# Performance work log

Measured on AMD Instinct MI355X. Metric: run time of the kernel, lower is better.

The kernel has to match this reference:

```python
import jax, jax.numpy as jnp
from jax import lax
import numpy as np

NPOINT = 2048
NSAMPLE = 16
LEAKY = 0.1


def _leaky(x):
    return jnp.where(x >= 0, x, LEAKY * x)


def _fps(pts, npoint):
    # pts: [B, N, 3] -> idx [B, npoint] (furthest point sampling, start at index 0)
    B, N, _ = pts.shape

    def step(carry, _):
        dist, far = carry  # dist [B,N], far [B]
        c = jnp.take_along_axis(pts, far[:, None, None], axis=1)  # [B,1,3]
        d = jnp.sum((pts - c) ** 2, -1)  # [B,N]
        dist = jnp.minimum(dist, d)
        nxt = jnp.argmax(dist, -1).astype(jnp.int32)
        return (dist, nxt), far

    init = (jnp.full((B, N), 1e10, pts.dtype), jnp.zeros((B,), jnp.int32))
    _, idx = lax.scan(step, init, None, length=npoint)
    return jnp.transpose(idx)  # [B, npoint]


def setup_inputs() -> dict:
    key = jax.random.key(0)
    ks = jax.random.split(key, 6)
    B, N, D, O = 8, 8192, 64, 128
    xyz = jax.random.normal(ks[0], (B, 3, N), jnp.float32)
    points = jax.random.normal(ks[1], (B, D, N), jnp.float32)
    W_kernel = jax.random.normal(ks[2], (O, D + 3), jnp.float32) * 0.05
    W_linear = jax.random.normal(ks[3], (O + NSAMPLE, O + NSAMPLE), jnp.float32) * 0.05
    W_point = jax.random.normal(ks[4], (NSAMPLE, NSAMPLE), jnp.float32) * 0.05
    W_channel = jax.random.normal(ks[5], (O, O), jnp.float32) * 0.05
    return {"xyz": xyz, "points": points, "W_kernel": W_kernel,
            "W_linear": W_linear, "W_point": W_point, "W_channel": W_channel}


def reference(xyz, points, W_kernel, W_linear, W_point, W_channel):
    K, S = NSAMPLE, NPOINT
    xyz_t = jnp.transpose(xyz, (0, 2, 1))      # [B,N,3]
    pts_t = jnp.transpose(points, (0, 2, 1))   # [B,N,D]

    fps_idx = _fps(xyz_t, S)                   # [B,S]
    new_xyz = jax.vmap(lambda p, i: p[i])(xyz_t, fps_idx)  # [B,S,3]

    # KNN: squared distances new_xyz -> xyz
    d = (jnp.sum(new_xyz ** 2, -1)[:, :, None]
         + jnp.sum(xyz_t ** 2, -1)[:, None, :]
         - 2.0 * jnp.einsum('bsc,bnc->bsn', new_xyz, xyz_t))  # [B,S,N]
    _, knn = lax.top_k(-d, K)                  # [B,S,K]

    gxyz = jax.vmap(lambda p, i: p[i])(xyz_t, knn)          # [B,S,K,3]
    gxyz_n = gxyz - new_xyz[:, :, None, :]
    gpts = jax.vmap(lambda p, i: p[i])(pts_t, knn)          # [B,S,K,D]
    new_points = jnp.concatenate([gxyz_n, gpts], -1)        # [B,S,K,3+D]

    # 1x1 conv2d kernel + LeakyReLU
    feat = _leaky(jnp.einsum('oc,bskc->bosk', W_kernel, new_points))  # [B,O,S,K]

    ch_avg = jnp.mean(feat, -1)                # [B,O,S]
    pt_avg = jnp.mean(feat, 1)                 # [B,S,K]
    agg = jnp.concatenate([ch_avg, jnp.transpose(pt_avg, (0, 2, 1))], 1)  # [B,O+K,S]
    agg = _leaky(jnp.einsum('oc,bcs->bos', W_linear, agg))

    wp = jax.nn.sigmoid(jnp.einsum('oc,bcs->bos', W_point, agg[:, -K:]))   # [B,K,S]
    wc = jax.nn.sigmoid(jnp.einsum('oc,bcs->bos', W_channel, agg[:, :-K]))  # [B,O,S]

    gated = feat * wc[:, :, :, None] * jnp.transpose(wp, (0, 2, 1))[:, None, :, :]
    out = jnp.mean(gated, -1)                  # [B,O,S]
    return jnp.transpose(new_xyz, (0, 2, 1)), out, fps_idx
```

## Files before the change

kernel.cpp:

```cpp
#include <hip/hip_runtime.h>
#include <stdint.h>

#define NB 8
#define NPT 8192
#define ND 64
#define NO 128
#define NS 2048
#define NK 16
#define NCONS 248
#define NITER 67

typedef float f32x2 __attribute__((ext_vector_type(2)));

constexpr int WS_PTS_T  = 0;
constexpr int WS_XYZW   = WS_PTS_T + NB*NPT*ND;
constexpr int WS_GFAR   = WS_XYZW + NB*NPT*4;
constexpr int WS_SYNC   = WS_GFAR + NB*NS;

constexpr int OUT_NEWXYZ = 0;
constexpr int OUT_FEAT   = NB*3*NS;
constexpr int OUT_FPS    = OUT_FEAT + NB*NO*NS;

__device__ __forceinline__ float sq3(float x, float y, float z) {
#pragma clang fp contract(off)
  return (x*x + y*y) + z*z;
}

__device__ __forceinline__ f32x2 fps_d2(f32x2 px, f32x2 py, f32x2 pz, f32x2 cx, f32x2 cy, f32x2 cz) {
#pragma clang fp contract(off)
  f32x2 dx = px - cx, dy = py - cy, dz = pz - cz;
  return (dx*dx + dy*dy) + dz*dz;
}

__device__ __forceinline__ float knn_d(float qn, float pn,
                                       float qx,float qy,float qz,
                                       float px,float py,float pz) {
#pragma clang fp contract(off)
  float dot = (qx*px + qy*py) + qz*pz;
  return (qn + pn) - 2.0f*dot;
}

#define DPP_STEP_F(x, ctrl, rm, bm, op) { \
  int _v = __builtin_amdgcn_update_dpp(__float_as_int(x), __float_as_int(x), ctrl, rm, bm, false); \
  x = op(x, __int_as_float(_v)); }

__device__ __forceinline__ float wave_max_dpp(float x) {
  DPP_STEP_F(x, 0x111, 0xF, 0xF, fmaxf)
  DPP_STEP_F(x, 0x112, 0xF, 0xF, fmaxf)
  DPP_STEP_F(x, 0x114, 0xF, 0xF, fmaxf)
  DPP_STEP_F(x, 0x118, 0xF, 0xF, fmaxf)
  DPP_STEP_F(x, 0x142, 0xA, 0xF, fmaxf)
  DPP_STEP_F(x, 0x143, 0xC, 0xF, fmaxf)
  return x;
}
__device__ __forceinline__ float dpp8_max(float x) {
  DPP_STEP_F(x, 0x111, 0xF, 0xF, fmaxf)
  DPP_STEP_F(x, 0x112, 0xF, 0xF, fmaxf)
  DPP_STEP_F(x, 0x114, 0xF, 0xF, fmaxf)
  return x;
}

__global__ void k_init(float* __restrict__ ws) {
  int idx = blockIdx.x*512 + threadIdx.x;
  if (idx < NB*NS) ((int*)(ws + WS_GFAR))[idx] = -1;
  if (idx < 32)    ((int*)(ws + WS_SYNC))[idx] = 0;
}

struct MegaShared {
  union {
    struct {
      float lxyz[NPT][4];
      unsigned long long wred[2][8];
      int tag[2][8];
    } f;
    struct { float tile[64][65]; } tr;
    struct {
      float W[128*69];
      union {
        float dist[NPT];
        struct { float np[16*69]; float ft[16*132]; float chred[256]; float ptred[16*17]; } p2;
      } u;
      unsigned long long kred[8];
      int selIdx[16];
      float agg[144];
      float a2[144];
      float gates[144];
      int farSlot;
    } c;
  } u;
};

__global__ __launch_bounds__(512) void k_mega(const float* __restrict__ xyz,
                                              const float* __restrict__ points,
                                              const float* __restrict__ Wkern,
                                              const float* __restrict__ Wlin,
                                              const float* __restrict__ Wpt,
                                              const float* __restrict__ Wch,
                                              float* __restrict__ ws,
                                              float* __restrict__ dout) {
  __shared__ MegaShared sh;
  const int bid = blockIdx.x, t = threadIdx.x;
  int* syncp = (int*)(ws + WS_SYNC);
  int* gfar  = (int*)(ws + WS_GFAR);

  if (bid < NB) {
    const float* xb = xyz + (size_t)bid*3*NPT;
    f32x2 px2[8], py2[8], pz2[8], dist2[8];
    const int base = t << 4;
    const int w = t >> 6;
#pragma unroll
    for (int jj = 0; jj < 4; jj++) {
      float4 vx = *reinterpret_cast<const float4*>(xb + base + jj*4);
      float4 vy = *reinterpret_cast<const float4*>(xb + NPT + base + jj*4);
      float4 vz = *reinterpret_cast<const float4*>(xb + 2*NPT + base + jj*4);
      px2[jj*2+0] = f32x2{vx.x, vx.y}; px2[jj*2+1] = f32x2{vx.z, vx.w};
      py2[jj*2+0] = f32x2{vy.x, vy.y}; py2[jj*2+1] = f32x2{vy.z, vy.w};
      pz2[jj*2+0] = f32x2{vz.x, vz.y}; pz2[jj*2+1] = f32x2{vz.z, vz.w};
      dist2[jj*2+0] = f32x2{1e10f, 1e10f}; dist2[jj*2+1] = f32x2{1e10f, 1e10f};
      float xs[4] = {vx.x, vx.y, vx.z, vx.w};
      float ys[4] = {vy.x, vy.y, vy.z, vy.w};
      float zs[4] = {vz.x, vz.y, vz.z, vz.w};
#pragma unroll
      for (int i = 0; i < 4; i++) {
        float4 rec; rec.x = xs[i]; rec.y = ys[i]; rec.z = zs[i]; rec.w = 0.f;
        *reinterpret_cast<float4*>(&sh.u.f.lxyz[base + jj*4 + i][0]) = rec;
      }
    }
    if (t < 16) sh.u.f.tag[t >> 3][t & 7] = 0;
    __syncthreads();

    int far = 0;
    int* gfb = gfar + (size_t)bid*NS;

    for (int s = 0; s < NS; s++) {
      if (t == 0)
        __hip_atomic_store(&gfb[s], far, __ATOMIC_RELAXED, __HIP_MEMORY_SCOPE_AGENT);

      const float4 c4 = *reinterpret_cast<const float4*>(&sh.u.f.lxyz[far][0]);
      const f32x2 c2x = {c4.x, c4.x}, c2y = {c4.y, c4.y}, c2z = {c4.z, c4.z};

      f32x2 vmax2 = {-1.0f, -1.0f};
#pragma unroll
      for (int j = 0; j < 8; j++) {
        f32x2 dd = fps_d2(px2[j], py2[j], pz2[j], c2x, c2y, c2z);
        f32x2 nd;
        nd.x = fminf(dist2[j].x, dd.x);
        nd.y = fminf(dist2[j].y, dd.y);
        dist2[j] = nd;
        vmax2.x = fmaxf(vmax2.x, nd.x);
        vmax2.y = fmaxf(vmax2.y, nd.y);
      }
      float bv = fmaxf(vmax2.x, vmax2.y);
      int bi = base;
#pragma unroll
      for (int j = 7; j >= 0; --j) {
        if (dist2[j].y == bv) bi = base + 2*j + 1;
        if (dist2[j].x == bv) bi = base + 2*j;
      }
      float wm = wave_max_dpp(bv);
      float wmax = __int_as_float(__builtin_amdgcn_readlane(__float_as_int(wm), 63));
      unsigned long long eq = __ballot(bv == wmax);
      int winner = __ffsll((unsigned long long)eq) - 1;
      int wbi = __builtin_amdgcn_readlane(bi, winner);

      const int par = s & 1;
      const int mytag = (s >> 1) + 1;
      if ((t & 63) == 0) {
        sh.u.f.wred[par][w] = ((unsigned long long)__float_as_uint(wmax) << 32) | (unsigned)wbi;
        __hip_atomic_store(&sh.u.f.tag[par][w], mytag, __ATOMIC_RELEASE, __HIP_MEMORY_SCOPE_WORKGROUP);
      }
      {
        int* tp = &sh.u.f.tag[par][t & 7];
        while (__hip_atomic_load(tp, __ATOMIC_ACQUIRE, __HIP_MEMORY_SCOPE_WORKGROUP) != mytag) {}
      }
      {
        unsigned long long kk = sh.u.f.wred[par][t & 7];
        float sv = __int_as_float((int)(unsigned)(kk >> 32));
        float sm = dpp8_max(sv);
        float M = __int_as_float(__builtin_amdgcn_readlane(__float_as_int(sm), 7));
        unsigned long long eqm = __ballot(sv == M) & 0xFFull;
        int wwin = __ffsll(eqm) - 1;
        far = __builtin_amdgcn_readlane((int)(kk & 0xFFFFFFFFull), wwin);
      }
    }
    return;
  }

  const int cbid = bid - NB;

  for (int tile = cbid; tile < 1024; tile += NCONS) {
    const int b  = tile >> 7;
    const int n0 = (tile & 127) << 6;
    const float* pb = points + (size_t)b*ND*NPT;
    {
      int dR = t >> 3, cg = t & 7;
      const float* src = pb + (size_t)dR*NPT + n0 + cg*8;
      float4 v0 = *reinterpret_cast<const float4*>(src);
      float4 v1 = *reinterpret_cast<const float4*>(src + 4);
      sh.u.tr.tile[dR][cg*8+0]=v0.x; sh.u.tr.tile[dR][cg*8+1]=v0.y;
      sh.u.tr.tile[dR][cg*8+2]=v0.z; sh.u.tr.tile[dR][cg*8+3]=v0.w;
      sh.u.tr.tile[dR][cg*8+4]=v1.x; sh.u.tr.tile[dR][cg*8+5]=v1.y;
      sh.u.tr.tile[dR][cg*8+6]=v1.z; sh.u.tr.tile[dR][cg*8+7]=v1.w;
    }
    __syncthreads();
    {
      int nl = t >> 3, dg = t & 7;
      float4 w0, w1;
      w0.x = sh.u.tr.tile[dg*8+0][nl]; w0.y = sh.u.tr.tile[dg*8+1][nl];
      w0.z = sh.u.tr.tile[dg*8+2][nl]; w0.w = sh.u.tr.tile[dg*8+3][nl];
      w1.x = sh.u.tr.tile[dg*8+4][nl]; w1.y = sh.u.tr.tile[dg*8+5][nl];
      w1.z = sh.u.tr.tile[dg*8+6][nl]; w1.w = sh.u.tr.tile[dg*8+7][nl];
      float* dst = ws + WS_PTS_T + ((size_t)b*NPT + n0 + nl)*ND + dg*8;
      *reinterpret_cast<float4*>(dst)     = w0;
      *reinterpret_cast<float4*>(dst + 4) = w1;
    }
    __syncthreads();
  }
  for (int chunk = cbid; chunk < 128; chunk += NCONS) {
    int g = chunk*512 + t;
    int b = g >> 13, n = g & 8191;
    const float* xb = xyz + (size_t)b*3*NPT;
    float x = xb[n], y = xb[NPT+n], z = xb[2*NPT+n];
    float4 v; v.x=x; v.y=y; v.z=z; v.w=sq3(x,y,z);
    *reinterpret_cast<float4*>(ws + WS_XYZW + (size_t)g*4) = v;
  }
  __syncthreads();
  if (t == 0) {
    __hip_atomic_fetch_add(&syncp[0], 1, __ATOMIC_ACQ_REL, __HIP_MEMORY_SCOPE_AGENT);
    while (__hip_atomic_load(&syncp[0], __ATOMIC_RELAXED, __HIP_MEMORY_SCOPE_AGENT) < NCONS)
      __builtin_amdgcn_s_sleep(8);
    (void)__hip_atomic_load(&syncp[0], __ATOMIC_ACQUIRE, __HIP_MEMORY_SCOPE_AGENT);
  }
  __syncthreads();

  for (int g = t; g < 128*67; g += 512) {
    int o = g / 67, c = g - o*67;
    sh.u.c.W[o*69+c] = Wkern[g];
  }
  __syncthreads();

  for (int j = 0; j < NITER; j++) {
    const int i = cbid + j*NCONS;
    const bool active = (i < NB*NS);
    const int ii = active ? i : (NB*NS - 1);
    const int b = ii & 7, s = ii >> 3;

    if (t == 0) {
      int f;
      while ((f = __hip_atomic_load(&gfar[(size_t)b*NS + s], __ATOMIC_RELAXED, __HIP_MEMORY_SCOPE_AGENT)) == -1)
        __builtin_amdgcn_s_sleep(8);
      sh.u.c.farSlot = f;
    }
    __syncthreads();
    const int far = sh.u.c.farSlot;

    const float* xyzw = ws + WS_XYZW + (size_t)b*NPT*4;
    const float4 q = *reinterpret_cast<const float4*>(xyzw + (size_t)far*4);

    if (active) {
      if (t == 3) dout[OUT_FPS + (size_t)b*NS + s] = (float)far;
      else if (t < 3) dout[OUT_NEWXYZ + (size_t)b*3*NS + (size_t)t*NS + s] = (t==0) ? q.x : (t==1) ? q.y : q.z;
    }

#pragma unroll
    for (int i2 = 0; i2 < 16; i2++) {
      int n = t + (i2 << 9);
      float4 p = *reinterpret_cast<const float4*>(xyzw + (size_t)n*4);
      sh.u.c.u.dist[n] = knn_d(q.w, p.w, q.x, q.y, q.z, p.x, p.y, p.z);
    }
    __syncthreads();

    for (int r = 0; r < NK; r++) {
      float bv = __int_as_float(0x7F800000); int bi = NPT;
#pragma unroll
      for (int i2 = 0; i2 < 16; i2++) {
        int n = t + (i2 << 9);
        float v = sh.u.c.u.dist[n];
        if (v < bv) { bv = v; bi = n; }
      }
      unsigned uu = __float_as_uint(bv);
      uu ^= ((unsigned)((int)uu >> 31)) | 0x80000000u;
      unsigned long long key = ((unsigned long long)uu << 32) | (unsigned)bi;
#pragma unroll
      for (int m = 1; m < 64; m <<= 1) {
        unsigned long long o = __shfl_xor(key, m, 64);
        key = (o < key) ? o : key;
      }
      if ((t & 63) == 0) sh.u.c.kred[t >> 6] = key;
      __syncthreads();
      if (t == 0) {
        unsigned long long kmin = sh.u.c.kred[0];
#pragma unroll
        for (int w2 = 1; w2 < 8; w2++) { unsigned long long o = sh.u.c.kred[w2]; if (o < kmin) kmin = o; }
        int win = (int)(kmin & 0xFFFFFFFFull);
        sh.u.c.selIdx[r] = win;
        sh.u.c.u.dist[win] = __int_as_float(0x7F800000);
      }
      __syncthreads();
    }

    if (t < 256) {
      int k = t >> 4, cg = t & 15;
      int idx = sh.u.c.selIdx[k];
      float4 f = *reinterpret_cast<const float4*>(ws + WS_PTS_T + ((size_t)b*NPT + idx)*ND + cg*4);
      float* nprow = sh.u.c.u.p2.np + k*69;
      nprow[3+cg*4+0]=f.x; nprow[3+cg*4+1]=f.y; nprow[3+cg*4+2]=f.z; nprow[3+cg*4+3]=f.w;
      if (cg == 0) {
        float4 g4 = *reinterpret_cast<const float4*>(xyzw + (size_t)idx*4);
        nprow[0]=g4.x-q.x; nprow[1]=g4.y-q.y; nprow[2]=g4.z-q.z;
      }
    }
    __syncthreads();

    if (t < 256) {
      const int o = t & 127, khalf = t >> 7, k0 = khalf*8;
      float acc[8] = {0,0,0,0,0,0,0,0};
      const float* Wrow = sh.u.c.W + o*69;
      for (int c = 0; c < 67; c++) {
        float wv = Wrow[c];
#pragma unroll
        for (int kk = 0; kk < 8; kk++)
          acc[kk] = fmaf(wv, sh.u.c.u.p2.np[(k0+kk)*69 + c], acc[kk]);
      }
      float chp = 0.f;
#pragma unroll
      for (int kk = 0; kk < 8; kk++) {
        float a = acc[kk]; a = (a >= 0.f) ? a : 0.1f*a;
        sh.u.c.u.p2.ft[(k0+kk)*132 + o] = a; chp += a;
      }
      sh.u.c.u.p2.chred[khalf*128 + o] = chp;
    }
    __syncthreads();

    if (t < 128) sh.u.c.agg[t] = (sh.u.c.u.p2.chred[t] + sh.u.c.u.p2.chred[128+t]) * 0.0625f;
    if (t < 256) {
      int k = t & 15, og = t >> 4;
      float pp = 0.f;
#pragma unroll
      for (int jj = 0; jj < 8; jj++) pp += sh.u.c.u.p2.ft[k*132 + og*8 + jj];
      sh.u.c.u.p2.ptred[k*17 + og] = pp;
    }
    __syncthreads();
    if (t < 16) {
      float pv = 0.f;
#pragma unroll
      for (int og = 0; og < 16; og++) pv += sh.u.c.u.p2.ptred[t*17 + og];
      sh.u.c.agg[128 + t] = pv * 0.0078125f;
    }
    __syncthreads();

    if (t < 144) {
      float a = 0.f;
      const float* wr = Wlin + t*144;
      for (int c = 0; c < 144; c++) a = fmaf(wr[c], sh.u.c.agg[c], a);
      sh.u.c.a2[t] = (a >= 0.f) ? a : 0.1f*a;
    }
    __syncthreads();

    if (t < 128) {
      float a = 0.f;
      const float* wr = Wch + t*128;
      for (int c = 0; c < 128; c++) a = fmaf(wr[c], sh.u.c.a2[c], a);
      sh.u.c.gates[t] = 1.f / (1.f + expf(-a));
    } else if (t < 144) {
      int o = t - 128;
      float a = 0.f;
      const float* wr = Wpt + o*16;
      for (int c = 0; c < 16; c++) a = fmaf(wr[c], sh.u.c.a2[128+c], a);
      sh.u.c.gates[t] = 1.f / (1.f + expf(-a));
    }
    __syncthreads();

    if (t < 128 && active) {
      float sum = 0.f;
#pragma unroll
      for (int k = 0; k < 16; k++)
        sum = fmaf(sh.u.c.u.p2.ft[k*132 + t], sh.u.c.gates[128 + k], sum);
      dout[OUT_FEAT + ((size_t)b*NO + t)*NS + s] = sum * sh.u.c.gates[t] * 0.0625f;
    }
    __syncthreads();
  }
}

extern "C" void kernel_launch(void* const* d_in, const int* in_sizes, int n_in,
                              void* d_out, int out_size, void* d_ws, size_t ws_size,
                              hipStream_t stream) {
  (void)in_sizes; (void)n_in; (void)out_size; (void)ws_size;
  const float* xyz    = (const float*)d_in[0];
  const float* points = (const float*)d_in[1];
  const float* Wk     = (const float*)d_in[2];
  const float* Wl     = (const float*)d_in[3];
  const float* Wp     = (const float*)d_in[4];
  const float* Wc     = (const float*)d_in[5];
  float* ws  = (float*)d_ws;
  float* out = (float*)d_out;

  hipLaunchKernelGGL(k_init, dim3(32), dim3(512), 0, stream, ws);

  void* args[] = { (void*)&xyz, (void*)&points, (void*)&Wk, (void*)&Wl,
                   (void*)&Wp, (void*)&Wc, (void*)&ws, (void*)&out };
  hipLaunchCooperativeKernel(reinterpret_cast<void*>(k_mega),
                             dim3(NB + NCONS), dim3(512), args, 0, stream);
}
```

Measured before the change: 1.992 ms.

## Streamline KNN top-k reduction and replace FPS tag spin with barrier

```diff
diff --git a/kernel.cpp b/kernel.cpp
--- a/kernel.cpp
+++ b/kernel.cpp
@@ -43,6 +43,9 @@
 #define DPP_STEP_F(x, ctrl, rm, bm, op) { \
   int _v = __builtin_amdgcn_update_dpp(__float_as_int(x), __float_as_int(x), ctrl, rm, bm, false); \
   x = op(x, __int_as_float(_v)); }
+#define DPP_STEP_U(x, ctrl, rm, cmp) { \
+  unsigned _v = (unsigned)__builtin_amdgcn_update_dpp((int)x, (int)x, ctrl, rm, 0xF, false); \
+  x = (_v cmp x) ? _v : x; }
 
 __device__ __forceinline__ float wave_max_dpp(float x) {
   DPP_STEP_F(x, 0x111, 0xF, 0xF, fmaxf)
@@ -53,6 +56,20 @@
   DPP_STEP_F(x, 0x143, 0xC, 0xF, fmaxf)
   return x;
 }
+__device__ __forceinline__ float wave_min_dpp(float x) {
+  DPP_STEP_F(x, 0x111, 0xF, 0xF, fminf)
+  DPP_STEP_F(x, 0x112, 0xF, 0xF, fminf)
+  DPP_STEP_F(x, 0x114, 0xF, 0xF, fminf)
+  DPP_STEP_F(x, 0x118, 0xF, 0xF, fminf)
+  DPP_STEP_F(x, 0x142, 0xA, 0xF, fminf)
+  DPP_STEP_F(x, 0x143, 0xC, 0xF, fminf)
+  return x;
+}
+__device__ __forceinline__ unsigned wave_umin_dpp(unsigned x) {
+  DPP_STEP_U(x, 0x111, 0xF, <) DPP_STEP_U(x, 0x112, 0xF, <) DPP_STEP_U(x, 0x114, 0xF, <)
+  DPP_STEP_U(x, 0x118, 0xF, <) DPP_STEP_U(x, 0x142, 0xA, <) DPP_STEP_U(x, 0x143, 0xC, <)
+  return x;
+}
 __device__ __forceinline__ float dpp8_max(float x) {
   DPP_STEP_F(x, 0x111, 0xF, 0xF, fmaxf)
   DPP_STEP_F(x, 0x112, 0xF, 0xF, fmaxf)
@@ -71,7 +88,6 @@
     struct {
       float lxyz[NPT][4];
       unsigned long long wred[2][8];
-      int tag[2][8];
     } f;
     struct { float tile[64][65]; } tr;
     struct {
@@ -80,8 +96,7 @@
         float dist[NPT];
         struct { float np[16*69]; float ft[16*132]; float chred[256]; float ptred[16*17]; } p2;
       } u;
-      unsigned long long kred[8];
-      int selIdx[16];
+      unsigned long long kred[2][8];
       float agg[144];
       float a2[144];
       float gates[144];
@@ -107,7 +122,6 @@
     const float* xb = xyz + (size_t)bid*3*NPT;
     f32x2 px2[8], py2[8], pz2[8], dist2[8];
     const int base = t << 4;
-    const int w = t >> 6;
 #pragma unroll
     for (int jj = 0; jj < 4; jj++) {
       float4 vx = *reinterpret_cast<const float4*>(xb + base + jj*4);
@@ -126,7 +140,6 @@
         *reinterpret_cast<float4*>(&sh.u.f.lxyz[base + jj*4 + i][0]) = rec;
       }
     }
-    if (t < 16) sh.u.f.tag[t >> 3][t & 7] = 0;
     __syncthreads();
 
     int far = 0;
@@ -162,17 +175,10 @@
       unsigned long long eq = __ballot(bv == wmax);
       int winner = __ffsll((unsigned long long)eq) - 1;
       int wbi = __builtin_amdgcn_readlane(bi, winner);
-
       const int par = s & 1;
-      const int mytag = (s >> 1) + 1;
-      if ((t & 63) == 0) {
-        sh.u.f.wred[par][w] = ((unsigned long long)__float_as_uint(wmax) << 32) | (unsigned)wbi;
-        __hip_atomic_store(&sh.u.f.tag[par][w], mytag, __ATOMIC_RELEASE, __HIP_MEMORY_SCOPE_WORKGROUP);
-      }
-      {
-        int* tp = &sh.u.f.tag[par][t & 7];
-        while (__hip_atomic_load(tp, __ATOMIC_ACQUIRE, __HIP_MEMORY_SCOPE_WORKGROUP) != mytag) {}
-      }
+      if ((t & 63) == 0)
+        sh.u.f.wred[par][t >> 6] = ((unsigned long long)__float_as_uint(wmax) << 32) | (unsigned)wbi;
+      __syncthreads();
       {
         unsigned long long kk = sh.u.f.wred[par][t & 7];
         float sv = __int_as_float((int)(unsigned)(kk >> 32));
@@ -239,6 +245,8 @@
   }
   __syncthreads();
 
+  const int myK = t >> 4;
+
   for (int j = 0; j < NITER; j++) {
     const int i = cbid + j*NCONS;
     const bool active = (i < NB*NS);
@@ -270,38 +278,43 @@
     }
     __syncthreads();
 
+    int exclWin = NPT;
+    int myIdx = 0;
     for (int r = 0; r < NK; r++) {
       float bv = __int_as_float(0x7F800000); int bi = NPT;
 #pragma unroll
       for (int i2 = 0; i2 < 16; i2++) {
         int n = t + (i2 << 9);
         float v = sh.u.c.u.dist[n];
-        if (v < bv) { bv = v; bi = n; }
-      }
-      unsigned uu = __float_as_uint(bv);
-      uu ^= ((unsigned)((int)uu >> 31)) | 0x80000000u;
-      unsigned long long key = ((unsigned long long)uu << 32) | (unsigned)bi;
-#pragma unroll
-      for (int m = 1; m < 64; m <<= 1) {
-        unsigned long long o = __shfl_xor(key, m, 64);
-        key = (o < key) ? o : key;
-      }
-      if ((t & 63) == 0) sh.u.c.kred[t >> 6] = key;
+        if (n != exclWin && v < bv) { bv = v; bi = n; }
+      }
+      float wmv = wave_min_dpp(bv);
+      float M = __int_as_float(__builtin_amdgcn_readlane(__float_as_int(wmv), 63));
+      unsigned cand = (bv == M) ? (unsigned)bi : 0xFFFFFFFFu;
+      unsigned wcv = wave_umin_dpp(cand);
+      unsigned widx = (unsigned)__builtin_amdgcn_readlane((int)wcv, 63);
+      if ((t & 63) == 0)
+        sh.u.c.kred[r & 1][t >> 6] = ((unsigned long long)__float_as_uint(M) << 32) | widx;
       __syncthreads();
-      if (t == 0) {
-        unsigned long long kmin = sh.u.c.kred[0];
-#pragma unroll
-        for (int w2 = 1; w2 < 8; w2++) { unsigned long long o = sh.u.c.kred[w2]; if (o < kmin) kmin = o; }
-        int win = (int)(kmin & 0xFFFFFFFFull);
-        sh.u.c.selIdx[r] = win;
-        sh.u.c.u.dist[win] = __int_as_float(0x7F800000);
-      }
-      __syncthreads();
+      unsigned long long k0 = sh.u.c.kred[r & 1][0];
+      float best = __int_as_float((int)(unsigned)(k0 >> 32));
+      unsigned bidx = (unsigned)(k0 & 0xFFFFFFFFull);
+#pragma unroll
+      for (int w2 = 1; w2 < 8; w2++) {
+        unsigned long long kk = sh.u.c.kred[r & 1][w2];
+        float v2 = __int_as_float((int)(unsigned)(kk >> 32));
+        unsigned ix = (unsigned)(kk & 0xFFFFFFFFull);
+        if (v2 < best || (v2 == best && ix < bidx)) { best = v2; bidx = ix; }
+      }
+      const int win = (int)bidx;
+      if (r == myK) myIdx = win;
+      if (r < NK-1 && (win & 511) == t) sh.u.c.u.dist[win] = __int_as_float(0x7F800000);
+      exclWin = win;
     }
 
     if (t < 256) {
-      int k = t >> 4, cg = t & 15;
-      int idx = sh.u.c.selIdx[k];
+      int k = myK, cg = t & 15;
+      int idx = myIdx;
       float4 f = *reinterpret_cast<const float4*>(ws + WS_PTS_T + ((size_t)b*NPT + idx)*ND + cg*4);
       float* nprow = sh.u.c.u.p2.np + k*69;
       nprow[3+cg*4+0]=f.x; nprow[3+cg*4+1]=f.y; nprow[3+cg*4+2]=f.z; nprow[3+cg*4+3]=f.w;
@@ -313,20 +326,20 @@
     __syncthreads();
 
     if (t < 256) {
-      const int o = t & 127, khalf = t >> 7, k0 = khalf*8;
+      const int o = t & 127, khalf = t >> 7, k0h = khalf*8;
       float acc[8] = {0,0,0,0,0,0,0,0};
       const float* Wrow = sh.u.c.W + o*69;
       for (int c = 0; c < 67; c++) {
         float wv = Wrow[c];
 #pragma unroll
         for (int kk = 0; kk < 8; kk++)
-          acc[kk] = fmaf(wv, sh.u.c.u.p2.np[(k0+kk)*69 + c], acc[kk]);
+          acc[kk] = fmaf(wv, sh.u.c.u.p2.np[(k0h+kk)*69 + c], acc[kk]);
       }
       float chp = 0.f;
 #pragma unroll
       for (int kk = 0; kk < 8; kk++) {
         float a = acc[kk]; a = (a >= 0.f) ? a : 0.1f*a;
-        sh.u.c.u.p2.ft[(k0+kk)*132 + o] = a; chp += a;
+        sh.u.c.u.p2.ft[(k0h+kk)*132 + o] = a; chp += a;
       }
       sh.u.c.u.p2.chred[khalf*128 + o] = chp;
     }
```

Measured after the change: 1.866 ms. 6.3% less time.
